# Kernel tuning notes

Measured on AMD Instinct MI355X. Metric: run time of the kernel, lower is better.

The kernel has to match this reference:

```python
import jax, jax.numpy as jnp
import numpy as np

TEMPERATURE = 12.5
SINK_EPS = 0.05   # entropic regularization for Sinkhorn (approximates exact EMD/LP)
SINK_ITERS = 50


def _l2norm(x, axis, eps):
    # matches F.normalize(p=2): x / max(||x||, eps)
    n = jnp.sqrt(jnp.sum(x * x, axis=axis, keepdims=True))
    return x / jnp.maximum(n, eps)


def get_weight_vector(A, B):
    # A: [b, M, c, h, w], B: [b, N, c, h, w] -> [b, M, N, h*w]
    b, M, c, h, w = A.shape
    Bn = _l2norm(B, axis=2, eps=1e-12)
    Bpool = Bn.mean(axis=(-2, -1))            # adaptive_avg_pool2d to 1x1 -> [b, N, c]
    An = _l2norm(A, axis=2, eps=1e-12)
    comb = jnp.einsum('bmchw,bnc->bmnhw', An, Bpool).reshape(b, M, Bpool.shape[1], h * w)
    return jax.nn.relu(comb) + 0.001


def get_similarity_map(proto, query):
    # proto: [b, W, c, h, w], query: [b, Q, c, h, w] -> [b, Q, W, hw_q, hw_p]
    b, W, c, h, w = proto.shape
    Q = query.shape[1]
    qf = query.reshape(b, Q, c, h * w)
    pf = proto.reshape(b, W, c, h * w)
    qn = _l2norm(qf, axis=2, eps=1e-8)        # cosine_similarity eps=1e-8 over channel dim
    pn = _l2norm(pf, axis=2, eps=1e-8)
    return jnp.einsum('bqcx,bwcy->bqwxy', qn, pn)


def sinkhorn_plan(cost, a, b):
    # cost: [..., n, m]; a: [..., n]; b: [..., m]  (a, b are probability masses)
    loga = jnp.log(a)
    logb = jnp.log(b)
    f0 = jnp.zeros_like(a)
    g0 = jnp.zeros_like(b)

    def body(_, fg):
        f, g = fg
        f = SINK_EPS * (loga - jax.nn.logsumexp((g[..., None, :] - cost) / SINK_EPS, axis=-1))
        g = SINK_EPS * (logb - jax.nn.logsumexp((f[..., :, None] - cost) / SINK_EPS, axis=-2))
        return (f, g)

    f, g = jax.lax.fori_loop(0, SINK_ITERS, body, (f0, g0))
    return jnp.exp((f[..., :, None] + g[..., None, :] - cost) / SINK_EPS)


def reference(query, proto, way, shot):
    # weight vectors: [b,Q,W,n] and [b,W,Q,n]
    weight_1 = get_weight_vector(query, proto)
    weight_2 = get_weight_vector(proto, query)
    sim = get_similarity_map(proto, query)          # [b, Q, W, n, n]
    n = sim.shape[-1]

    a = weight_1 / weight_1.sum(-1, keepdims=True)  # row masses (query nodes)
    w2 = jnp.transpose(weight_2, (0, 2, 1, 3))      # [b, Q, W, n] (weight_2[k, j, i] pairing)
    bm = w2 / w2.sum(-1, keepdims=True)             # col masses (proto nodes)

    cost = 1.0 - sim
    # Original detaches the cost and solves EMD on CPU (cv2); flow is a constant wrt autograd.
    plan = jax.lax.stop_gradient(sinkhorn_plan(cost, a, bm)) * n  # cv2 total mass = num_node

    temperature = TEMPERATURE / n
    logits = (sim * plan).sum((-1, -2)) * temperature  # [b, Q, W]
    return logits


def setup_inputs() -> dict:
    key = jax.random.key(0)
    k1, k2 = jax.random.split(key)
    query = jax.random.normal(k1, (8, 75, 640, 8, 8), dtype=jnp.float32)
    proto = jax.random.normal(k2, (8, 5, 640, 8, 8), dtype=jnp.float32)
    return {"query": query, "proto": proto, "way": 5, "shot": 1}
```

## Files before the change

kernel.cpp:

```cpp
#include <hip/hip_runtime.h>
#include <hip/hip_bf16.h>

typedef __attribute__((ext_vector_type(8))) short short8;
typedef __attribute__((ext_vector_type(4))) float f32x4;
typedef __attribute__((ext_vector_type(2))) float f32x2;

#define SEPS   0.05f
#define KC     28.853900817779268f
#define EPSLN2 0.034657359027997264f
#define LN2    0.6931471805599453f

__device__ __forceinline__ unsigned short bf16_rne(float f) {
  unsigned int u = __float_as_uint(f);
  unsigned int r = (u + 0x7fffu + ((u >> 16) & 1u)) >> 16;
  return (unsigned short)r;
}

__global__ __launch_bounds__(1024) void norm_pack(const float* __restrict__ q,
                                                  const float* __restrict__ p,
                                                  unsigned short* __restrict__ qo,
                                                  unsigned short* __restrict__ po) {
  int blk = blockIdx.x;
  const float* src;
  unsigned short* dst;
  if (blk < 600) { src = q + (size_t)blk * 40960; dst = qo + (size_t)blk * 40960; }
  else           { src = p + (size_t)(blk - 600) * 40960; dst = po + (size_t)(blk - 600) * 40960; }

  int t = threadIdx.x;
  int xg = t & 15, cg = t >> 4;
  int x4 = xg * 4;

  f32x4 v[10];
  float ss[4] = {0.f, 0.f, 0.f, 0.f};
  #pragma unroll
  for (int k = 0; k < 10; ++k) {
    v[k] = *(const f32x4*)(src + (size_t)(cg + 64 * k) * 64 + x4);
    #pragma unroll
    for (int j = 0; j < 4; ++j) ss[j] = fmaf(v[k][j], v[k][j], ss[j]);
  }

  #pragma unroll
  for (int j = 0; j < 4; ++j) {
    ss[j] += __shfl_xor(ss[j], 16, 64);
    ss[j] += __shfl_xor(ss[j], 32, 64);
  }
  __shared__ float red[16][64];
  __shared__ float scale_s[64];
  int wv = t >> 6, ln = t & 63;
  if (ln < 16) {
    #pragma unroll
    for (int j = 0; j < 4; ++j) red[wv][ln * 4 + j] = ss[j];
  }
  __syncthreads();
  if (t < 64) {
    float s = 0.f;
    #pragma unroll
    for (int w2 = 0; w2 < 16; ++w2) s += red[w2][t];
    scale_s[t] = 1.0f / fmaxf(sqrtf(s), 1e-12f);
  }
  __syncthreads();
  float sc[4];
  #pragma unroll
  for (int j = 0; j < 4; ++j) sc[j] = scale_s[x4 + j];

  __shared__ float tile[2][64][65];
  int t9 = t & 511, th = t >> 9;
  int pr = t9 >> 3, pc = (t9 & 7) * 8;
  #pragma unroll
  for (int rd = 0; rd < 5; ++rd) {
    #pragma unroll
    for (int h = 0; h < 2; ++h) {
      f32x4 u = v[rd * 2 + h];
      #pragma unroll
      for (int j = 0; j < 4; ++j) tile[h][x4 + j][cg] = u[j] * sc[j];
    }
    __syncthreads();
    unsigned int pk[4];
    #pragma unroll
    for (int k2 = 0; k2 < 4; ++k2) {
      unsigned int lo = bf16_rne(tile[th][pr][pc + 2 * k2]);
      unsigned int hi = bf16_rne(tile[th][pr][pc + 2 * k2 + 1]);
      pk[k2] = lo | (hi << 16);
    }
    *(uint4*)(dst + (size_t)pr * 640 + (rd * 2 + th) * 64 + pc) = make_uint4(pk[0], pk[1], pk[2], pk[3]);
    __syncthreads();
  }
}

__device__ __forceinline__ float rl(float v, int lane) {
  return __int_as_float(__builtin_amdgcn_readlane(__float_as_int(v), lane));
}
__device__ __forceinline__ long pack2(float v, int j) {
  unsigned int lo = (unsigned int)__builtin_amdgcn_readlane(__float_as_int(v), j);
  unsigned int hi = (unsigned int)__builtin_amdgcn_readlane(__float_as_int(v), j + 1);
  return (long)(((unsigned long long)hi << 32) | lo);
}
__device__ __forceinline__ float wredsum(float v) {
  #pragma unroll
  for (int m = 1; m < 64; m <<= 1) v += __shfl_xor(v, m, 64);
  return v;
}
#define SWZ(row) ((((row) ^ ((row) >> 3)) & 15) << 2)

__global__ __launch_bounds__(64, 2) void gemm_sink(const unsigned short* __restrict__ A,
                                                   const unsigned short* __restrict__ B,
                                                   float* __restrict__ out) {
  __shared__ alignas(16) char sh[8192];
  unsigned short (*As)[64][32] = (unsigned short (*)[64][32])sh;
  float* Cm = (float*)sh;

  int blk0 = blockIdx.x;
  int blk = (blk0 & 7) * 375 + (blk0 >> 3);
  int w = blk % 5;
  int bq = blk / 5;
  int b = bq / 75;
  const unsigned short* Ab = A + (size_t)bq * 40960;
  const unsigned short* Bb = B + (size_t)(b * 5 + w) * 40960;

  int l = threadIdx.x;
  int lrow = l >> 2, lslot = l & 3;
  int fr = l & 15, k8 = l >> 4;
  int soff = ((k8 ^ (fr & 3)) << 4);

  f32x4 acc[4][4];
  #pragma unroll
  for (int i = 0; i < 4; ++i)
    #pragma unroll
    for (int j = 0; j < 4; ++j)
      acc[i][j] = (f32x4){0.f, 0.f, 0.f, 0.f};

  auto stageA = [&](int buf, int k0) {
    #pragma unroll
    for (int t = 0; t < 4; ++t) {
      int row = t * 16 + lrow;
      int sl = lslot ^ (row & 3);
      __builtin_amdgcn_global_load_lds(
          (const __attribute__((address_space(1))) unsigned int*)(Ab + (size_t)row * 640 + k0 + sl * 8),
          (__attribute__((address_space(3))) unsigned int*)&As[buf][t * 16][0], 16, 0, 0);
    }
  };
  short8 bF0[4], bF1[4];
  auto loadB = [&](short8* dst, int k0) {
    #pragma unroll
    for (int mi = 0; mi < 4; ++mi)
      dst[mi] = *(const short8*)(Bb + (size_t)(mi * 16 + fr) * 640 + k0 + k8 * 8);
  };
  auto compute = [&](int buf, const short8* bFr) {
    short8 aF[4];
    #pragma unroll
    for (int mi = 0; mi < 4; ++mi)
      aF[mi] = *(const short8*)((const char*)&As[buf][0][0] + ((mi * 16 + fr) * 64 + soff));
    #pragma unroll
    for (int mi = 0; mi < 4; ++mi)
      #pragma unroll
      for (int ni = 0; ni < 4; ++ni)
        acc[mi][ni] = __builtin_amdgcn_mfma_f32_16x16x32_bf16(aF[mi], bFr[ni], acc[mi][ni], 0, 0, 0);
  };

  stageA(0, 0);
  loadB(bF0, 0);
  #pragma unroll 1
  for (int s2 = 0; s2 < 10; ++s2) {
    int se = s2 * 2;
    stageA(1, (se + 1) * 32);
    loadB(bF1, (se + 1) * 32);
    asm volatile("s_waitcnt vmcnt(8)" ::: "memory");
    compute(0, bF0);
    int so = se + 1;
    if (so < 19) {
      stageA(0, (so + 1) * 32);
      loadB(bF0, (so + 1) * 32);
      asm volatile("s_waitcnt vmcnt(8)" ::: "memory");
    } else {
      asm volatile("s_waitcnt vmcnt(0)" ::: "memory");
    }
    compute(1, bF1);
  }

  f32x2 EcolP[32], ErowP[32];
  float colsum = 0.f, rowsum = 0.f;
  #pragma unroll
  for (int ch = 0; ch < 2; ++ch) {
    #pragma unroll
    for (int mh = 0; mh < 2; ++mh) {
      int mi = ch * 2 + mh;
      #pragma unroll
      for (int ni = 0; ni < 4; ++ni)
        #pragma unroll
        for (int r = 0; r < 4; ++r) {
          int rr = mh * 16 + k8 * 4 + r;
          int col = ni * 16 + fr;
          Cm[rr * 64 + (col ^ SWZ(rr))] = 1.0f - acc[mi][ni][r];
        }
    }
    asm volatile("s_waitcnt lgkmcnt(0)" ::: "memory");
    __builtin_amdgcn_sched_barrier(0);
    #pragma unroll
    for (int i2 = 0; i2 < 16; ++i2) {
      float c0 = Cm[(2 * i2) * 64 + (l ^ SWZ(2 * i2))];
      float c1 = Cm[(2 * i2 + 1) * 64 + (l ^ SWZ(2 * i2 + 1))];
      colsum += (1.0f - c0);
      colsum += (1.0f - c1);
      EcolP[ch * 16 + i2][0] = __builtin_amdgcn_exp2f(-KC * c0);
      EcolP[ch * 16 + i2][1] = __builtin_amdgcn_exp2f(-KC * c1);
    }
    if ((l >> 5) == ch) {
      int rr = l & 31, sw = SWZ(rr);
      #pragma unroll
      for (int j4 = 0; j4 < 16; ++j4) {
        f32x4 cc = *(const f32x4*)&Cm[rr * 64 + ((j4 * 4) ^ sw)];
        rowsum += cc[0]; rowsum += cc[1]; rowsum += cc[2]; rowsum += cc[3];
        ErowP[j4 * 2][0]     = __builtin_amdgcn_exp2f(-KC * cc[0]);
        ErowP[j4 * 2][1]     = __builtin_amdgcn_exp2f(-KC * cc[1]);
        ErowP[j4 * 2 + 1][0] = __builtin_amdgcn_exp2f(-KC * cc[2]);
        ErowP[j4 * 2 + 1][1] = __builtin_amdgcn_exp2f(-KC * cc[3]);
      }
    }
    asm volatile("s_waitcnt lgkmcnt(0)" ::: "memory");
    __builtin_amdgcn_sched_barrier(0);
  }

  float w1 = fmaxf(1.0f - rowsum * (1.0f / 64.0f), 0.f) + 0.001f;
  float w2 = fmaxf(colsum * (1.0f / 64.0f), 0.f) + 0.001f;
  float amass = w1 * __builtin_amdgcn_rcpf(wredsum(w1));
  float bmass = w2 * __builtin_amdgcn_rcpf(wredsum(w2));

  const float UMIN = 1.80485139e-35f;
  const float UMAX = 5.54062238e+34f;

  float uu = 0.f, vv = 1.0f;
  float pv = vv;
  #pragma unroll 1
  for (int it = 0; it < 50; ++it) {
    f32x2 sA0 = {1e-37f, 0.f}, sA1 = {0.f, 0.f}, sA2 = {0.f, 0.f}, sA3 = {0.f, 0.f};
    #pragma unroll
    for (int g = 0; g < 4; ++g) {
      long P[8];
      #pragma unroll
      for (int p = 0; p < 8; ++p) P[p] = pack2(vv, (g * 8 + p) * 2);
      #pragma unroll
      for (int p = 0; p < 8; ++p) {
        if ((p & 3) == 0)      asm("v_pk_fma_f32 %0, %1, %2, %0" : "+v"(sA0) : "v"(ErowP[g * 8 + p]), "s"(P[p]));
        else if ((p & 3) == 1) asm("v_pk_fma_f32 %0, %1, %2, %0" : "+v"(sA1) : "v"(ErowP[g * 8 + p]), "s"(P[p]));
        else if ((p & 3) == 2) asm("v_pk_fma_f32 %0, %1, %2, %0" : "+v"(sA2) : "v"(ErowP[g * 8 + p]), "s"(P[p]));
        else                   asm("v_pk_fma_f32 %0, %1, %2, %0" : "+v"(sA3) : "v"(ErowP[g * 8 + p]), "s"(P[p]));
      }
    }
    float s = ((sA0[0] + sA0[1]) + (sA1[0] + sA1[1])) + ((sA2[0] + sA2[1]) + (sA3[0] + sA3[1]));
    uu = fminf(fmaxf(amass * __builtin_amdgcn_rcpf(s), UMIN), UMAX);

    f32x2 tA0 = {1e-37f, 0.f}, tA1 = {0.f, 0.f}, tA2 = {0.f, 0.f}, tA3 = {0.f, 0.f};
    #pragma unroll
    for (int g = 0; g < 4; ++g) {
      long P[8];
      #pragma unroll
      for (int p = 0; p < 8; ++p) P[p] = pack2(uu, (g * 8 + p) * 2);
      #pragma unroll
      for (int p = 0; p < 8; ++p) {
        if ((p & 3) == 0)      asm("v_pk_fma_f32 %0, %1, %2, %0" : "+v"(tA0) : "v"(EcolP[g * 8 + p]), "s"(P[p]));
        else if ((p & 3) == 1) asm("v_pk_fma_f32 %0, %1, %2, %0" : "+v"(tA1) : "v"(EcolP[g * 8 + p]), "s"(P[p]));
        else if ((p & 3) == 2) asm("v_pk_fma_f32 %0, %1, %2, %0" : "+v"(tA2) : "v"(EcolP[g * 8 + p]), "s"(P[p]));
        else                   asm("v_pk_fma_f32 %0, %1, %2, %0" : "+v"(tA3) : "v"(EcolP[g * 8 + p]), "s"(P[p]));
      }
    }
    float t = ((tA0[0] + tA0[1]) + (tA1[0] + tA1[1])) + ((tA2[0] + tA2[1]) + (tA3[0] + tA3[1]));
    vv = fminf(fmaxf(bmass * __builtin_amdgcn_rcpf(t), UMIN), UMAX);

    if (__all(fabsf(vv - pv) <= 1e-5f * vv)) break;
    pv = vv;
  }

  float a1 = 0.f, a2 = 0.f;
  #pragma unroll
  for (int g = 0; g < 8; ++g) {
    float vj[8];
    #pragma unroll
    for (int p = 0; p < 8; ++p) vj[p] = rl(vv, g * 8 + p);
    #pragma unroll
    for (int p = 0; p < 8; ++p) {
      int j = g * 8 + p;
      float Ej = ErowP[j >> 1][j & 1];
      float e = fminf((uu * Ej) * vj[p], 1.32922800e36f);
      float c = -EPSLN2 * __builtin_amdgcn_logf(Ej);
      a1 += e;
      a2 = fmaf(c, e, a2);
    }
  }
  float tot = wredsum(a1 - a2);
  if (l == 0) out[blk] = 12.5f * tot;
}

extern "C" void kernel_launch(void* const* d_in, const int* in_sizes, int n_in,
                              void* d_out, int out_size, void* d_ws, size_t ws_size,
                              hipStream_t stream) {
  const float* query = (const float*)d_in[0];
  const float* proto = (const float*)d_in[1];
  float* out = (float*)d_out;
  char* ws = (char*)d_ws;

  const size_t A_OFF = 0;
  const size_t B_OFF = 49152000;
  if (ws_size < 52428800ull) return;

  unsigned short* Abf = (unsigned short*)(ws + A_OFF);
  unsigned short* Bbf = (unsigned short*)(ws + B_OFF);

  norm_pack<<<640, 1024, 0, stream>>>(query, proto, Abf, Bbf);
  gemm_sink<<<3000, 64, 0, stream>>>(Abf, Bbf, out);
}
```

Measured before the change: 77.32 us.

## Keep row exp-kernel matrix in LDS instead of registers during Sinkhorn

Writes the full 64x64 cost tile to a 16KB LDS buffer with a new XOR swizzle, then overwrites it in place with the row-wise exp kernel, instead of holding ErowP in 64 VGPRs. The row-update half of each Sinkhorn iteration now reads its operands from LDS, as does the final reduction. This cuts register pressure and removes the two-chunk staging pass, but adds LDS reads inside the 50-iteration loop and doubles the shared memory footprint.

```diff
diff --git a/kernel.cpp b/kernel.cpp
--- a/kernel.cpp
+++ b/kernel.cpp
@@ -100,14 +100,14 @@
   for (int m = 1; m < 64; m <<= 1) v += __shfl_xor(v, m, 64);
   return v;
 }
-#define SWZ(row) ((((row) ^ ((row) >> 3)) & 15) << 2)
+#define SL(row, j4) (((row) << 6) + ((((j4) ^ ((row) & 15))) << 2))
 
 __global__ __launch_bounds__(64, 2) void gemm_sink(const unsigned short* __restrict__ A,
                                                    const unsigned short* __restrict__ B,
                                                    float* __restrict__ out) {
-  __shared__ alignas(16) char sh[8192];
+  __shared__ alignas(16) char sh[16384];
   unsigned short (*As)[64][32] = (unsigned short (*)[64][32])sh;
-  float* Cm = (float*)sh;
+  float* Em = (float*)sh;
 
   int blk0 = blockIdx.x;
   int blk = (blk0 & 7) * 375 + (blk0 >> 3);
@@ -177,48 +177,46 @@
     compute(1, bF1);
   }
 
-  f32x2 EcolP[32], ErowP[32];
+  int crow = k8 * 4;
+  #pragma unroll
+  for (int mi = 0; mi < 4; ++mi)
+    #pragma unroll
+    for (int ni = 0; ni < 4; ++ni)
+      #pragma unroll
+      for (int r = 0; r < 4; ++r) {
+        int rr = mi * 16 + crow + r;
+        int col = ni * 16 + fr;
+        Em[SL(rr, col >> 2) + (col & 3)] = 1.0f - acc[mi][ni][r];
+      }
+  asm volatile("s_waitcnt lgkmcnt(0)" ::: "memory");
+  __builtin_amdgcn_sched_barrier(0);
+
+  f32x2 EcolP[32];
   float colsum = 0.f, rowsum = 0.f;
-  #pragma unroll
-  for (int ch = 0; ch < 2; ++ch) {
-    #pragma unroll
-    for (int mh = 0; mh < 2; ++mh) {
-      int mi = ch * 2 + mh;
-      #pragma unroll
-      for (int ni = 0; ni < 4; ++ni)
-        #pragma unroll
-        for (int r = 0; r < 4; ++r) {
-          int rr = mh * 16 + k8 * 4 + r;
-          int col = ni * 16 + fr;
-          Cm[rr * 64 + (col ^ SWZ(rr))] = 1.0f - acc[mi][ni][r];
-        }
-    }
-    asm volatile("s_waitcnt lgkmcnt(0)" ::: "memory");
-    __builtin_amdgcn_sched_barrier(0);
-    #pragma unroll
-    for (int i2 = 0; i2 < 16; ++i2) {
-      float c0 = Cm[(2 * i2) * 64 + (l ^ SWZ(2 * i2))];
-      float c1 = Cm[(2 * i2 + 1) * 64 + (l ^ SWZ(2 * i2 + 1))];
-      colsum += (1.0f - c0);
-      colsum += (1.0f - c1);
-      EcolP[ch * 16 + i2][0] = __builtin_amdgcn_exp2f(-KC * c0);
-      EcolP[ch * 16 + i2][1] = __builtin_amdgcn_exp2f(-KC * c1);
-    }
-    if ((l >> 5) == ch) {
-      int rr = l & 31, sw = SWZ(rr);
-      #pragma unroll
-      for (int j4 = 0; j4 < 16; ++j4) {
-        f32x4 cc = *(const f32x4*)&Cm[rr * 64 + ((j4 * 4) ^ sw)];
-        rowsum += cc[0]; rowsum += cc[1]; rowsum += cc[2]; rowsum += cc[3];
-        ErowP[j4 * 2][0]     = __builtin_amdgcn_exp2f(-KC * cc[0]);
-        ErowP[j4 * 2][1]     = __builtin_amdgcn_exp2f(-KC * cc[1]);
-        ErowP[j4 * 2 + 1][0] = __builtin_amdgcn_exp2f(-KC * cc[2]);
-        ErowP[j4 * 2 + 1][1] = __builtin_amdgcn_exp2f(-KC * cc[3]);
-      }
-    }
-    asm volatile("s_waitcnt lgkmcnt(0)" ::: "memory");
-    __builtin_amdgcn_sched_barrier(0);
-  }
+  int l4 = l >> 2, lm = l & 3;
+  #pragma unroll
+  for (int i2 = 0; i2 < 32; ++i2) {
+    float c0 = Em[SL(2 * i2, l4) + lm];
+    float c1 = Em[SL(2 * i2 + 1, l4) + lm];
+    colsum += (1.0f - c0);
+    colsum += (1.0f - c1);
+    EcolP[i2][0] = __builtin_amdgcn_exp2f(-KC * c0);
+    EcolP[i2][1] = __builtin_amdgcn_exp2f(-KC * c1);
+  }
+  #pragma unroll
+  for (int j4 = 0; j4 < 16; ++j4) {
+    f32x4* rp = (f32x4*)&Em[SL(l, j4)];
+    f32x4 cc = *rp;
+    rowsum += cc[0]; rowsum += cc[1]; rowsum += cc[2]; rowsum += cc[3];
+    f32x4 e;
+    e[0] = __builtin_amdgcn_exp2f(-KC * cc[0]);
+    e[1] = __builtin_amdgcn_exp2f(-KC * cc[1]);
+    e[2] = __builtin_amdgcn_exp2f(-KC * cc[2]);
+    e[3] = __builtin_amdgcn_exp2f(-KC * cc[3]);
+    *rp = e;
+  }
+  asm volatile("s_waitcnt lgkmcnt(0)" ::: "memory");
+  __builtin_amdgcn_sched_barrier(0);
 
   float w1 = fmaxf(1.0f - rowsum * (1.0f / 64.0f), 0.f) + 0.001f;
   float w2 = fmaxf(colsum * (1.0f / 64.0f), 0.f) + 0.001f;
@@ -238,13 +236,18 @@
       long P[8];
       #pragma unroll
       for (int p = 0; p < 8; ++p) P[p] = pack2(vv, (g * 8 + p) * 2);
-      #pragma unroll
-      for (int p = 0; p < 8; ++p) {
-        if ((p & 3) == 0)      asm("v_pk_fma_f32 %0, %1, %2, %0" : "+v"(sA0) : "v"(ErowP[g * 8 + p]), "s"(P[p]));
-        else if ((p & 3) == 1) asm("v_pk_fma_f32 %0, %1, %2, %0" : "+v"(sA1) : "v"(ErowP[g * 8 + p]), "s"(P[p]));
-        else if ((p & 3) == 2) asm("v_pk_fma_f32 %0, %1, %2, %0" : "+v"(sA2) : "v"(ErowP[g * 8 + p]), "s"(P[p]));
-        else                   asm("v_pk_fma_f32 %0, %1, %2, %0" : "+v"(sA3) : "v"(ErowP[g * 8 + p]), "s"(P[p]));
-      }
+      const f32x2* q0 = (const f32x2*)&Em[SL(l, g * 4 + 0)];
+      const f32x2* q1 = (const f32x2*)&Em[SL(l, g * 4 + 1)];
+      const f32x2* q2 = (const f32x2*)&Em[SL(l, g * 4 + 2)];
+      const f32x2* q3 = (const f32x2*)&Em[SL(l, g * 4 + 3)];
+      asm("v_pk_fma_f32 %0, %1, %2, %0" : "+v"(sA0) : "v"(q0[0]), "s"(P[0]));
+      asm("v_pk_fma_f32 %0, %1, %2, %0" : "+v"(sA1) : "v"(q0[1]), "s"(P[1]));
+      asm("v_pk_fma_f32 %0, %1, %2, %0" : "+v"(sA2) : "v"(q1[0]), "s"(P[2]));
+      asm("v_pk_fma_f32 %0, %1, %2, %0" : "+v"(sA3) : "v"(q1[1]), "s"(P[3]));
+      asm("v_pk_fma_f32 %0, %1, %2, %0" : "+v"(sA0) : "v"(q2[0]), "s"(P[4]));
+      asm("v_pk_fma_f32 %0, %1, %2, %0" : "+v"(sA1) : "v"(q2[1]), "s"(P[5]));
+      asm("v_pk_fma_f32 %0, %1, %2, %0" : "+v"(sA2) : "v"(q3[0]), "s"(P[6]));
+      asm("v_pk_fma_f32 %0, %1, %2, %0" : "+v"(sA3) : "v"(q3[1]), "s"(P[7]));
     }
     float s = ((sA0[0] + sA0[1]) + (sA1[0] + sA1[1])) + ((sA2[0] + sA2[1]) + (sA3[0] + sA3[1]));
     uu = fminf(fmaxf(amass * __builtin_amdgcn_rcpf(s), UMIN), UMAX);
@@ -268,6 +271,7 @@
 
     if (__all(fabsf(vv - pv) <= 1e-5f * vv)) break;
     pv = vv;
+    asm volatile("" ::: "memory");
   }
 
   float a1 = 0.f, a2 = 0.f;
@@ -279,7 +283,7 @@
     #pragma unroll
     for (int p = 0; p < 8; ++p) {
       int j = g * 8 + p;
-      float Ej = ErowP[j >> 1][j & 1];
+      float Ej = Em[SL(l, j >> 2) + (j & 3)];
       float e = fminf((uu * Ej) * vj[p], 1.32922800e36f);
       float c = -EPSLN2 * __builtin_amdgcn_logf(Ej);
       a1 += e;
```

Result: slower. 84.35 us (+9.1%).
